# Kernel tuning notes

Hardware: AMD Instinct MI355X
Metric: run time of the kernel (lower is better)

## Reference

```python
import jax, jax.numpy as jnp
import numpy as np


def setup_inputs() -> dict:
    key = jax.random.key(0)
    kq, ks, kr, kx, ky = jax.random.split(key, 5)
    B, C, H, W, K = 2, 64, 128, 256, 32
    Q = jax.random.normal(kq, (B, C, H, W), dtype=jnp.float32)
    S = jax.random.normal(ks, (B, C, H, W), dtype=jnp.float32)
    R = jax.random.normal(kr, (B, C, H, W), dtype=jnp.float32)
    Pos_x = jax.random.randint(kx, (H * W, K), 0, H, dtype=jnp.int64 if jax.config.jax_enable_x64 else jnp.int32)
    Pos_y = jax.random.randint(ky, (H * W, K), 0, W, dtype=jnp.int64 if jax.config.jax_enable_x64 else jnp.int32)
    return {"Q": Q, "S": S, "R": R, "Pos_x": Pos_x, "Pos_y": Pos_y}


def reference(Q, S, R, Pos_x, Pos_y):
    B, C, H, W = Q.shape
    N = H * W
    px = Pos_x.reshape(-1)  # [N*K]
    py = Pos_y.reshape(-1)
    K = px.shape[0] // N
    # Gather keys/values at candidate positions: [B, C, N*K] -> [B, C, N, K]
    Key = S[:, :, px, py].reshape(B, C, N, K)
    Value = R[:, :, px, py].reshape(B, C, N, K)
    # Queries: [B, N, C]
    Qf = Q.reshape(B, C, N).transpose(0, 2, 1)
    # Per-pixel scores over K candidates (NO 1/sqrt(d) scaling, as in original)
    score = jnp.einsum('bnc,bcnk->bnk', Qf, Key)
    attn = jax.nn.softmax(score, axis=-1)
    # Attention-weighted sum of values: [B, N, C]
    out = jnp.einsum('bnk,bcnk->bnc', attn, Value)
    return out.reshape(B, H, W, C).transpose(0, 3, 1, 2)
```

## Files before the change

kernel.cpp:

```cpp
#include <hip/hip_runtime.h>
#include <hip/hip_fp16.h>

constexpr int B = 2, C = 64, H = 128, W = 256, N = H * W, K = 32;

typedef _Float16 hf2 __attribute__((ext_vector_type(2)));

template <int CTRL>
__device__ __forceinline__ float dppf(float x) {
    int i = __builtin_bit_cast(int, x);
    int r = __builtin_amdgcn_update_dpp(i, i, CTRL, 0xF, 0xF, false);
    return __builtin_bit_cast(float, r);
}

__global__ __launch_bounds__(256) void transpose_to_h(
    const float* __restrict__ Q, const float* __restrict__ S,
    const float* __restrict__ R,
    __half* __restrict__ Qt, __half* __restrict__ St, __half* __restrict__ Rt) {
    __shared__ float tile[C][65];
    const int n0 = blockIdx.x * 64;
    const int b  = blockIdx.y;
    const int z  = blockIdx.z;
    const float* src = (z == 0 ? S : (z == 1 ? R : Q)) + (size_t)b * C * N;
    __half2* d2 = (__half2*)((z == 0 ? St : (z == 1 ? Rt : Qt)) +
                             (size_t)b * N * C);
    {
        const int j = threadIdx.x & 63, c0 = threadIdx.x >> 6;
        const float* s = src + n0 + j;
#pragma unroll
        for (int r = 0; r < 16; ++r) {
            int c = c0 + r * 4;
            tile[c][j] = s[(size_t)c * N];
        }
    }
    __syncthreads();
    {
        const int c2 = threadIdx.x & 31, j0 = threadIdx.x >> 5;
#pragma unroll
        for (int r = 0; r < 8; ++r) {
            int j = j0 + 8 * r;
            d2[(size_t)(n0 + j) * 32 + c2] =
                __floats2half2_rn(tile[2 * c2][j], tile[2 * c2 + 1][j]);
        }
    }
}

__global__ __launch_bounds__(512, 8) void fepam_attn(
    const __half* __restrict__ Qt,
    const int* __restrict__ Px, const int* __restrict__ Py,
    const __half* __restrict__ St, const __half* __restrict__ Rt,
    float* __restrict__ Out) {
    __shared__ __align__(16) float ot[64][66];
    __shared__ __align__(16) unsigned aidx[8][8][32];

    const int tid  = threadIdx.x;
    const int lane = tid & 63;
    const int wave = tid >> 6;
    const int bx   = blockIdx.x;
    const int b    = bx & 1;
    const int n0   = (bx >> 1) * 64;

    const __half* Qtb = Qt + (size_t)b * N * C;
    const __half* Stb = St + (size_t)b * N * C;
    const __half* Rtb = Rt + (size_t)b * N * C;

    const int k = lane & 31;
    const int h = lane >> 5;
#pragma unroll 2
    for (int p = 0; p < 8; ++p) {
        const int n = n0 + wave * 8 + p;

        const int px  = Px[(size_t)n * K + k];
        const int py  = Py[(size_t)n * K + k];
        const int idx = px * W + py;

        const float4* kp = (const float4*)(Stb + (size_t)idx * C + h * 32);
        const float4* qp = (const float4*)(Qtb + (size_t)n * C + h * 32);
        float s = 0.f;
#pragma unroll
        for (int i = 0; i < 4; ++i) {
            float4 kraw = kp[i];
            float4 qraw = qp[i];
            const hf2* k2 = (const hf2*)&kraw;
            const hf2* q2 = (const hf2*)&qraw;
#pragma unroll
            for (int u = 0; u < 4; ++u)
                s = __builtin_amdgcn_fdot2(k2[u], q2[u], s, false);
        }
        s += __shfl_xor(s, 32);

        float m = s;
        m = fmaxf(m, dppf<0xB1>(m));
        m = fmaxf(m, dppf<0x4E>(m));
        m = fmaxf(m, dppf<0x141>(m));
        m = fmaxf(m, dppf<0x140>(m));
        m = fmaxf(m, __shfl_xor(m, 16));
        float e = __expf(s - m);
        float l = e;
        l += dppf<0xB1>(l);
        l += dppf<0x4E>(l);
        l += dppf<0x141>(l);
        l += dppf<0x140>(l);
        l += __shfl_xor(l, 16);
        const float a = e / l;

        if (lane < 32)
            aidx[wave][p][k] = ((unsigned)idx << 16) |
                               (unsigned)__half_as_ushort(__float2half_rn(a));
    }

    const int c2 = lane & 31;
    const int kh = lane >> 5;
    for (int p = 0; p < 8; ++p) {
        const int j = wave * 8 + p;
        float accx = 0.f, accy = 0.f;
#pragma unroll
        for (int g = 0; g < 8; ++g) {
            const uint4 pk4 = *(const uint4*)&aidx[wave][p][4 * g];
            const unsigned ua = kh ? pk4.z : pk4.x;
            const unsigned ub = kh ? pk4.w : pk4.y;
#pragma unroll
            for (int t = 0; t < 2; ++t) {
                const unsigned u = t ? ub : ua;
                const float a = __half2float(__ushort_as_half((unsigned short)(u & 0xffffu)));
                const __half2 v =
                    *(const __half2*)(Rtb + ((size_t)(u >> 16) << 6) + 2 * c2);
                const float2 vf = __half22float2(v);
                accx = fmaf(a, vf.x, accx);
                accy = fmaf(a, vf.y, accy);
            }
        }
        accx += __shfl_xor(accx, 32);
        accy += __shfl_xor(accy, 32);
        if (lane < 32)
            *(float2*)&ot[j][2 * c2] = make_float2(accx, accy);
    }
    __syncthreads();

    {
        const int j = tid & 63, c0 = tid >> 6;
        float* od = Out + (size_t)b * C * N + n0 + j;
#pragma unroll
        for (int r = 0; r < 8; ++r) {
            int c = c0 + r * 8;
            od[(size_t)c * N] = ot[j][c];
        }
    }
}

extern "C" void kernel_launch(void* const* d_in, const int* in_sizes, int n_in,
                              void* d_out, int out_size, void* d_ws, size_t ws_size,
                              hipStream_t stream) {
    const float* Q  = (const float*)d_in[0];
    const float* S  = (const float*)d_in[1];
    const float* R  = (const float*)d_in[2];
    const int*   Px = (const int*)d_in[3];
    const int*   Py = (const int*)d_in[4];
    float* Out = (float*)d_out;

    __half* St = (__half*)d_ws;
    __half* Rt = St + (size_t)B * N * C;
    __half* Qt = Rt + (size_t)B * N * C;

    dim3 tgrid(N / 64, B, 3);
    transpose_to_h<<<tgrid, 256, 0, stream>>>(Q, S, R, Qt, St, Rt);

    dim3 agrid(N / 64 * B);
    fepam_attn<<<agrid, 512, 0, stream>>>(Qt, Px, Py, St, Rt, Out);
}
```

Before: 154.2 us.

## Precompute 16-bit gather indices and restructure attention with 8-lane row gathers

```diff
diff --git a/kernel.cpp b/kernel.cpp
--- a/kernel.cpp
+++ b/kernel.cpp
@@ -12,14 +12,30 @@
     return __builtin_bit_cast(float, r);
 }
 
-__global__ __launch_bounds__(256) void transpose_to_h(
+__global__ __launch_bounds__(256) void fepam_prep(
     const float* __restrict__ Q, const float* __restrict__ S,
     const float* __restrict__ R,
-    __half* __restrict__ Qt, __half* __restrict__ St, __half* __restrict__ Rt) {
-    __shared__ float tile[C][65];
+    const int* __restrict__ Px, const int* __restrict__ Py,
+    __half* __restrict__ Qt, __half* __restrict__ St, __half* __restrict__ Rt,
+    unsigned short* __restrict__ Idx) {
     const int n0 = blockIdx.x * 64;
     const int b  = blockIdx.y;
     const int z  = blockIdx.z;
+
+    if (z == 3) {
+        if (b) return;
+#pragma unroll
+        for (int t = 0; t < 8; ++t) {
+            const int e  = threadIdx.x + 256 * t;
+            const int nl = e >> 5, k = e & 31;
+            const int n  = n0 + nl;
+            const int idx = Px[(size_t)n * K + k] * W + Py[(size_t)n * K + k];
+            Idx[(size_t)n * K + (k & 7) * 4 + (k >> 3)] = (unsigned short)idx;
+        }
+        return;
+    }
+
+    __shared__ float tile[C][65];
     const float* src = (z == 0 ? S : (z == 1 ? R : Q)) + (size_t)b * C * N;
     __half2* d2 = (__half2*)((z == 0 ? St : (z == 1 ? Rt : Qt)) +
                              (size_t)b * N * C);
@@ -45,12 +61,10 @@
 }
 
 __global__ __launch_bounds__(512, 8) void fepam_attn(
-    const __half* __restrict__ Qt,
-    const int* __restrict__ Px, const int* __restrict__ Py,
+    const __half* __restrict__ Qt, const unsigned short* __restrict__ Idx,
     const __half* __restrict__ St, const __half* __restrict__ Rt,
     float* __restrict__ Out) {
     __shared__ __align__(16) float ot[64][66];
-    __shared__ __align__(16) unsigned aidx[8][8][32];
 
     const int tid  = threadIdx.x;
     const int lane = tid & 63;
@@ -59,80 +73,94 @@
     const int b    = bx & 1;
     const int n0   = (bx >> 1) * 64;
 
+    const int c_oct = lane & 7;
+    const int k_loc = lane >> 3;
+    const bool hi8  = (lane & 8)  != 0;
+    const bool hi16 = (lane & 16) != 0;
+    const bool hi32 = (lane & 32) != 0;
+
     const __half* Qtb = Qt + (size_t)b * N * C;
     const __half* Stb = St + (size_t)b * N * C;
     const __half* Rtb = Rt + (size_t)b * N * C;
 
-    const int k = lane & 31;
-    const int h = lane >> 5;
 #pragma unroll 2
     for (int p = 0; p < 8; ++p) {
-        const int n = n0 + wave * 8 + p;
+        const int j = wave * 8 + p;
+        const int n = n0 + j;
 
-        const int px  = Px[(size_t)n * K + k];
-        const int py  = Py[(size_t)n * K + k];
-        const int idx = px * W + py;
+        const float4 qraw = *(const float4*)(Qtb + (size_t)n * C + c_oct * 8);
+        const ushort4 iv = *(const ushort4*)(Idx + (size_t)n * K + k_loc * 4);
+        const int idxg[4] = {iv.x, iv.y, iv.z, iv.w};
 
-        const float4* kp = (const float4*)(Stb + (size_t)idx * C + h * 32);
-        const float4* qp = (const float4*)(Qtb + (size_t)n * C + h * 32);
-        float s = 0.f;
+        float s[4];
+#pragma unroll
+        for (int g = 0; g < 4; ++g) {
+            const float4 kraw =
+                *(const float4*)(Stb + ((size_t)idxg[g] << 6) + c_oct * 8);
+            const hf2* k2 = (const hf2*)&kraw;
+            const hf2* q2 = (const hf2*)&qraw;
+            float acc = 0.f;
+#pragma unroll
+            for (int u = 0; u < 4; ++u)
+                acc = __builtin_amdgcn_fdot2(k2[u], q2[u], acc, false);
+            s[g] = acc;
+        }
+#pragma unroll
+        for (int g = 0; g < 4; ++g) {
+            s[g] += dppf<0xB1>(s[g]);
+            s[g] += dppf<0x4E>(s[g]);
+            s[g] += dppf<0x141>(s[g]);
+        }
+
+        float m = fmaxf(fmaxf(s[0], s[1]), fmaxf(s[2], s[3]));
+        m = fmaxf(m, dppf<0x128>(m));
+        m = fmaxf(m, __shfl_xor(m, 16));
+        m = fmaxf(m, __shfl_xor(m, 32));
+        float e0 = __expf(s[0] - m), e1 = __expf(s[1] - m);
+        float e2 = __expf(s[2] - m), e3 = __expf(s[3] - m);
+        float l = (e0 + e1) + (e2 + e3);
+        l += dppf<0x128>(l);
+        l += __shfl_xor(l, 16);
+        l += __shfl_xor(l, 32);
+        const float inv = 1.0f / l;
+        const float a[4] = {e0 * inv, e1 * inv, e2 * inv, e3 * inv};
+
+        float acc[8] = {0, 0, 0, 0, 0, 0, 0, 0};
+#pragma unroll
+        for (int g = 0; g < 4; ++g) {
+            const float4 vraw =
+                *(const float4*)(Rtb + ((size_t)idxg[g] << 6) + c_oct * 8);
+            const __half2* v2 = (const __half2*)&vraw;
+            const float ag = a[g];
+#pragma unroll
+            for (int u = 0; u < 4; ++u) {
+                const float2 vf = __half22float2(v2[u]);
+                acc[2 * u]     = fmaf(ag, vf.x, acc[2 * u]);
+                acc[2 * u + 1] = fmaf(ag, vf.y, acc[2 * u + 1]);
+            }
+        }
+
+        float r4[4];
 #pragma unroll
         for (int i = 0; i < 4; ++i) {
-            float4 kraw = kp[i];
-            float4 qraw = qp[i];
-            const hf2* k2 = (const hf2*)&kraw;
-            const hf2* q2 = (const hf2*)&qraw;
+            const float send = hi8 ? acc[i] : acc[4 + i];
+            const float recv = dppf<0x128>(send);
+            r4[i] = (hi8 ? acc[4 + i] : acc[i]) + recv;
+        }
+        float r2[2];
 #pragma unroll
-            for (int u = 0; u < 4; ++u)
-                s = __builtin_amdgcn_fdot2(k2[u], q2[u], s, false);
+        for (int i = 0; i < 2; ++i) {
+            const float send = hi16 ? r4[i] : r4[2 + i];
+            const float recv = __shfl_xor(send, 16);
+            r2[i] = (hi16 ? r4[2 + i] : r4[i]) + recv;
         }
-        s += __shfl_xor(s, 32);
-
-        float m = s;
-        m = fmaxf(m, dppf<0xB1>(m));
-        m = fmaxf(m, dppf<0x4E>(m));
-        m = fmaxf(m, dppf<0x141>(m));
-        m = fmaxf(m, dppf<0x140>(m));
-        m = fmaxf(m, __shfl_xor(m, 16));
-        float e = __expf(s - m);
-        float l = e;
-        l += dppf<0xB1>(l);
-        l += dppf<0x4E>(l);
-        l += dppf<0x141>(l);
-        l += dppf<0x140>(l);
-        l += __shfl_xor(l, 16);
-        const float a = e / l;
-
-        if (lane < 32)
-            aidx[wave][p][k] = ((unsigned)idx << 16) |
-                               (unsigned)__half_as_ushort(__float2half_rn(a));
-    }
-
-    const int c2 = lane & 31;
-    const int kh = lane >> 5;
-    for (int p = 0; p < 8; ++p) {
-        const int j = wave * 8 + p;
-        float accx = 0.f, accy = 0.f;
-#pragma unroll
-        for (int g = 0; g < 8; ++g) {
-            const uint4 pk4 = *(const uint4*)&aidx[wave][p][4 * g];
-            const unsigned ua = kh ? pk4.z : pk4.x;
-            const unsigned ub = kh ? pk4.w : pk4.y;
-#pragma unroll
-            for (int t = 0; t < 2; ++t) {
-                const unsigned u = t ? ub : ua;
-                const float a = __half2float(__ushort_as_half((unsigned short)(u & 0xffffu)));
-                const __half2 v =
-                    *(const __half2*)(Rtb + ((size_t)(u >> 16) << 6) + 2 * c2);
-                const float2 vf = __half22float2(v);
-                accx = fmaf(a, vf.x, accx);
-                accy = fmaf(a, vf.y, accy);
-            }
+        {
+            const float send = hi32 ? r2[0] : r2[1];
+            const float recv = __shfl_xor(send, 32);
+            const float r1   = (hi32 ? r2[1] : r2[0]) + recv;
+            const int c = c_oct * 8 + (hi8 ? 4 : 0) + (hi16 ? 2 : 0) + (hi32 ? 1 : 0);
+            ot[j][c] = r1;
         }
-        accx += __shfl_xor(accx, 32);
-        accy += __shfl_xor(accy, 32);
-        if (lane < 32)
-            *(float2*)&ot[j][2 * c2] = make_float2(accx, accy);
     }
     __syncthreads();
 
@@ -160,10 +188,11 @@
     __half* St = (__half*)d_ws;
     __half* Rt = St + (size_t)B * N * C;
     __half* Qt = Rt + (size_t)B * N * C;
+    unsigned short* Idx = (unsigned short*)(Qt + (size_t)B * N * C);
 
-    dim3 tgrid(N / 64, B, 3);
-    transpose_to_h<<<tgrid, 256, 0, stream>>>(Q, S, R, Qt, St, Rt);
+    dim3 pgrid(N / 64, B, 4);
+    fepam_prep<<<pgrid, 256, 0, stream>>>(Q, S, R, Px, Py, Qt, St, Rt, Idx);
 
     dim3 agrid(N / 64 * B);
-    fepam_attn<<<agrid, 512, 0, stream>>>(Qt, Px, Py, St, Rt, Out);
+    fepam_attn<<<agrid, 512, 0, stream>>>(Qt, Idx, St, Rt, Out);
 }
```

Result: no change. 155.2 us (+0.6%).
